# Kernel tuning notes

Measured on AMD Instinct MI355X. Metric: run time of the kernel, lower is better.

Reference implementation:

```python
import jax, jax.numpy as jnp
import numpy as np

LAT_MIN, LAT_MAX = -90.0, 90.0
LON_MIN, LON_MAX = 0.0, 360.0
N_LEVELS = 4
N_FEAT = 2
FINEST = 0.25
BASE = 1.0
LAT_SHAPE, LON_SHAPE = 720, 1440
GEODESIC_WEIGHT = True
TABLE = (LAT_SHAPE + 1) * (LON_SHAPE + 1)  # 1038961
# corner offsets in the torch BOX_OFFSETS order: (0,0),(0,1),(1,0),(1,1)
OFFS = np.array([[0, 0], [0, 1], [1, 0], [1, 1]], dtype=np.int32)


def setup_inputs() -> dict:
    key = jax.random.key(0)
    k1, k2 = jax.random.split(key)
    B = 2_000_000
    u = jax.random.uniform(k1, (B, 2), dtype=jnp.float32)
    # lat in [-90, 90), lon in [0, 360)
    x = jnp.stack([u[:, 0] * 180.0 - 90.0, u[:, 1] * 360.0], axis=1)
    embeddings = jax.random.uniform(k2, (N_LEVELS, TABLE, N_FEAT),
                                    minval=-1e-4, maxval=1e-4, dtype=jnp.float32)
    return {"x": x, "embeddings": embeddings}


def _geodesic(lat1, lon1, lat2, lon2):
    r = jnp.pi / 180.0
    rl1, rl2 = lat1 * r, lat2 * r
    dlat = (lat2 - lat1) * r
    dlon = (lon2 - lon1) * r
    a = jnp.sin(dlat / 2) ** 2 + jnp.cos(rl1) * jnp.cos(rl2) * jnp.sin(dlon / 2) ** 2
    return 2.0 * jnp.arctan2(jnp.sqrt(a), jnp.sqrt(1.0 - a))


def reference(x, embeddings):
    box_min = jnp.array([LAT_MIN - FINEST, LON_MIN - FINEST], dtype=x.dtype)
    box_max = jnp.array([LAT_MAX + FINEST, LON_MAX + FINEST], dtype=x.dtype)
    xc = jnp.clip(x, box_min, box_max)  # clamped coords used for grid indexing
    offs = jnp.asarray(OFFS)
    outs = []
    for i in range(N_LEVELS):
        gs = BASE * (2.0 ** i)  # grid size (same for lat and lon)
        bl = jnp.floor((xc - box_min) / gs).astype(jnp.int32)  # [B,2] bottom-left idx
        gmin = bl.astype(x.dtype) * gs + box_min                # [B,2]
        gmax = gmin + gs
        width = int(np.floor(LON_SHAPE / gs))
        # 4 corner flat indices: lat_idx * width + lon_idx -> [B,4]
        idx = (bl[:, 0:1] + offs[None, :, 0]) * width + (bl[:, 1:2] + offs[None, :, 1])
        e = embeddings[i][idx]  # gather: [B,4,F]
        if GEODESIC_WEIGHT:
            wlat = _geodesic(gmin[:, 0], gmin[:, 1], x[:, 0], gmin[:, 1]) / \
                   _geodesic(gmin[:, 0], gmin[:, 1], gmax[:, 0], gmin[:, 1])
            wlon = _geodesic(gmin[:, 0], x[:, 1], gmin[:, 0], gmax[:, 1]) / \
                   _geodesic(gmin[:, 0], gmin[:, 1], gmin[:, 0], gmax[:, 1])
        else:
            w = (x - gmin) / (gmax - gmin)
            wlat, wlon = w[:, 0], w[:, 1]
        # bilinear blend (corner order: 0=(0,0) 1=(0,1) 2=(1,0) 3=(1,1))
        c0 = e[:, 0] * (1 - wlat[:, None]) + e[:, 2] * wlat[:, None]
        c1 = e[:, 1] * (1 - wlat[:, None]) + e[:, 3] * wlat[:, None]
        outs.append(c0 * (1 - wlon[:, None]) + c1 * wlon[:, None])
    return jnp.concatenate(outs, axis=-1)  # [B, N_LEVELS*N_FEAT]
```

## Files before the change

kernel.cpp:

```cpp
#include <hip/hip_runtime.h>
#include <hip/hip_fp16.h>

#define NT 256

constexpr int TABLE_SZ = 721 * 1441;

constexpr int QLAT = 181, QLON = 361;
constexpr int NCELLS = QLAT * QLON;

constexpr int LUT_OFF0 = 0, LUT_OFF1 = 181, LUT_OFF2 = 272, LUT_OFF3 = 318;
constexpr int LUT_N = 341;

typedef float v4f __attribute__((ext_vector_type(4)));
typedef float v2f __attribute__((ext_vector_type(2)));

__device__ __constant__ float c_s2_tab[4] = {0.008726535498f, 0.017452406437f,
                                             0.034899496703f, 0.069756473744f};

__global__ __launch_bounds__(256)
void build_superquad(const float* __restrict__ emb, uint4* __restrict__ sq)
{
    int c = blockIdx.x * 256 + threadIdx.x;
    if (c >= NCELLS) return;
    int la = c / QLON, lo = c - la * QLON;
    const float2* embv = (const float2*)emb;
    #pragma unroll
    for (int i = 0; i < 4; ++i) {
        const int width = 1440 >> i;
        const int ra = la >> i, co = lo >> i;
        const float2* t = embv + (size_t)i * TABLE_SZ;
        float2 e0 = t[ra * width + co];
        float2 e1 = t[ra * width + co + 1];
        float2 e2 = t[(ra + 1) * width + co];
        float2 e3 = t[(ra + 1) * width + co + 1];
        union { uint4 u; __half2 h[4]; } pk;
        pk.h[0] = __floats2half2_rn(e0.x, e0.y);
        pk.h[1] = __floats2half2_rn(e1.x, e1.y);
        pk.h[2] = __floats2half2_rn(e2.x, e2.y);
        pk.h[3] = __floats2half2_rn(e3.x, e3.y);
        sq[(size_t)c * 4 + i] = pk.u;
    }
}

template <bool USE_SQ>
__global__ __launch_bounds__(NT)
void ngp_interp_kernel(const float* __restrict__ x,
                       const float* __restrict__ emb,
                       const uint4* __restrict__ sq,
                       float* __restrict__ out,
                       int B)
{
    const float r = 0.017453292519943295f;
    const float bmin_lat = -90.25f;
    const float bmin_lon = -0.25f;

    __shared__ float2 lut[LUT_N];
    for (int t = threadIdx.x; t < LUT_N; t += NT) {
        int lvl, row;
        if (t < LUT_OFF1)      { lvl = 0; row = t; }
        else if (t < LUT_OFF2) { lvl = 1; row = t - LUT_OFF1; }
        else if (t < LUT_OFF3) { lvl = 2; row = t - LUT_OFF2; }
        else                   { lvl = 3; row = t - LUT_OFF3; }
        const float gs = (float)(1 << lvl);
        const float gmin_lat = (float)row * gs + bmin_lat;
        const float ca = fabsf(__cosf(gmin_lat * r));
        const float z2 = ca * c_s2_tab[lvl];
        const float n2 = z2 + z2 * z2 * z2 * (1.0f / 6.0f);
        lut[t] = make_float2(ca, __builtin_amdgcn_rcpf(n2));
    }
    __syncthreads();

    const int p = blockIdx.x * NT + threadIdx.x;
    if (p >= B) return;

    const v2f xp = __builtin_nontemporal_load(reinterpret_cast<const v2f*>(x) + p);
    const float xlat = xp.x;
    const float xlon = xp.y;

    const float bmax_lat = 90.25f, bmax_lon = 360.25f;
    const float xc_lat = fminf(fmaxf(xlat, bmin_lat), bmax_lat);
    const float xc_lon = fminf(fmaxf(xlon, bmin_lon), bmax_lon);

    const float v_lat = xc_lat - bmin_lat;
    const float v_lon = xc_lon - bmin_lon;

    const int cell0 = (int)floorf(v_lat) * QLON + (int)floorf(v_lon);
    const uint4* cellp = sq + (size_t)cell0 * 4;

    const int lut_off[4] = {LUT_OFF0, LUT_OFF1, LUT_OFF2, LUT_OFF3};

    float o[8];

    #pragma unroll
    for (int i = 0; i < 4; ++i) {
        const float gs     = (float)(1 << i);
        const float inv_gs = 1.0f / gs;
        const int   width  = 1440 >> i;

        const float blat_f = floorf(v_lat * inv_gs);
        const float blon_f = floorf(v_lon * inv_gs);
        const float gmin_lat = blat_f * gs + bmin_lat;
        const float gmin_lon = blon_f * gs + bmin_lon;
        const float gmax_lon = gmin_lon + gs;
        const int bl_lat = (int)blat_f;

        v2f E0, E1, E2, E3;
        if (USE_SQ) {
            union { uint4 u; __half2 h[4]; } pk;
            pk.u = cellp[i];
            float2 f0 = __half22float2(pk.h[0]);
            float2 f1 = __half22float2(pk.h[1]);
            float2 f2 = __half22float2(pk.h[2]);
            float2 f3 = __half22float2(pk.h[3]);
            E0 = (v2f){f0.x, f0.y}; E1 = (v2f){f1.x, f1.y};
            E2 = (v2f){f2.x, f2.y}; E3 = (v2f){f3.x, f3.y};
        } else {
            const int bl_lon = (int)blon_f;
            const int idx00 = bl_lat * width + bl_lon;
            const float* base0 = emb + ((size_t)i * TABLE_SZ + (size_t)idx00) * 2;
            const float* base1 = base0 + (size_t)width * 2;
            v4f eA, eB;
            __builtin_memcpy(&eA, base0, 16);
            __builtin_memcpy(&eB, base1, 16);
            E0 = (v2f){eA.x, eA.y}; E1 = (v2f){eA.z, eA.w};
            E2 = (v2f){eB.x, eB.y}; E3 = (v2f){eB.z, eB.w};
        }

        const float wlat = (xlat - gmin_lat) * inv_gs;

        const float2 cl = lut[lut_off[i] + bl_lat];
        const float h1 = (gmax_lon - xlon) * r * 0.5f;
        const float s1 = h1 - h1 * h1 * h1 * (1.0f / 6.0f);
        const float z1 = cl.x * s1;
        const float n1 = z1 + z1 * z1 * z1 * (1.0f / 6.0f);
        const float wlon = n1 * cl.y;

        const v2f wa = {wlat, wlat};
        const v2f wo = {wlon, wlon};
        const v2f c0 = E0 + (E2 - E0) * wa;
        const v2f c1 = E1 + (E3 - E1) * wa;
        const v2f res = c0 + (c1 - c0) * wo;
        o[2*i]   = res.x;
        o[2*i+1] = res.y;
    }

    v4f* op = reinterpret_cast<v4f*>(out + (size_t)p * 8);
    v4f lo = {o[0], o[1], o[2], o[3]};
    v4f hi = {o[4], o[5], o[6], o[7]};
    __builtin_nontemporal_store(lo, op);
    __builtin_nontemporal_store(hi, op + 1);
}

extern "C" void kernel_launch(void* const* d_in, const int* in_sizes, int n_in,
                              void* d_out, int out_size, void* d_ws, size_t ws_size,
                              hipStream_t stream)
{
    const float* x   = (const float*)d_in[0];
    const float* emb = (const float*)d_in[1];
    float* out = (float*)d_out;
    const int B = in_sizes[0] / 2;
    const int grid = (B + NT - 1) / NT;

    const size_t sq_bytes = (size_t)NCELLS * 64;
    if (ws_size >= sq_bytes) {
        uint4* sq = (uint4*)d_ws;
        build_superquad<<<(NCELLS + 255) / 256, 256, 0, stream>>>(emb, sq);
        ngp_interp_kernel<true><<<grid, NT, 0, stream>>>(x, emb, sq, out, B);
    } else {
        ngp_interp_kernel<false><<<grid, NT, 0, stream>>>(x, emb, nullptr, out, B);
    }
}
```

Before: 123.3 us.

## Process two points per thread and parallelize superquad build per level

The build kernel now uses one thread per (cell, level) pair instead of looping over four levels per cell, so writes are coalesced across consecutive threads and there are more threads to work with. The main kernel handles two points per thread: it issues all eight 16-byte superquad loads up front for more memory-level parallelism, halves the number of blocks and the shared LUT setup per point, and writes four vector stores per thread. The old templated fallback is split out into its own kernel that computes the cosines inline. The trade-off is higher register pressure and a requirement that B be even.

```diff
diff --git a/kernel.cpp b/kernel.cpp
--- a/kernel.cpp
+++ b/kernel.cpp
@@ -20,32 +20,28 @@
 __global__ __launch_bounds__(256)
 void build_superquad(const float* __restrict__ emb, uint4* __restrict__ sq)
 {
-    int c = blockIdx.x * 256 + threadIdx.x;
-    if (c >= NCELLS) return;
-    int la = c / QLON, lo = c - la * QLON;
-    const float2* embv = (const float2*)emb;
-    #pragma unroll
-    for (int i = 0; i < 4; ++i) {
-        const int width = 1440 >> i;
-        const int ra = la >> i, co = lo >> i;
-        const float2* t = embv + (size_t)i * TABLE_SZ;
-        float2 e0 = t[ra * width + co];
-        float2 e1 = t[ra * width + co + 1];
-        float2 e2 = t[(ra + 1) * width + co];
-        float2 e3 = t[(ra + 1) * width + co + 1];
-        union { uint4 u; __half2 h[4]; } pk;
-        pk.h[0] = __floats2half2_rn(e0.x, e0.y);
-        pk.h[1] = __floats2half2_rn(e1.x, e1.y);
-        pk.h[2] = __floats2half2_rn(e2.x, e2.y);
-        pk.h[3] = __floats2half2_rn(e3.x, e3.y);
-        sq[(size_t)c * 4 + i] = pk.u;
-    }
-}
-
-template <bool USE_SQ>
+    int t = blockIdx.x * 256 + threadIdx.x;
+    if (t >= NCELLS * 4) return;
+    const int c = t >> 2;
+    const int i = t & 3;
+    const int la = c / QLON, lo = c - la * QLON;
+    const int width = 1440 >> i;
+    const int ra = la >> i, co = lo >> i;
+    const float2* tb = (const float2*)emb + (size_t)i * TABLE_SZ;
+    float2 e0 = tb[ra * width + co];
+    float2 e1 = tb[ra * width + co + 1];
+    float2 e2 = tb[(ra + 1) * width + co];
+    float2 e3 = tb[(ra + 1) * width + co + 1];
+    union { uint4 u; __half2 h[4]; } pk;
+    pk.h[0] = __floats2half2_rn(e0.x, e0.y);
+    pk.h[1] = __floats2half2_rn(e1.x, e1.y);
+    pk.h[2] = __floats2half2_rn(e2.x, e2.y);
+    pk.h[3] = __floats2half2_rn(e3.x, e3.y);
+    sq[t] = pk.u;
+}
+
 __global__ __launch_bounds__(NT)
 void ngp_interp_kernel(const float* __restrict__ x,
-                       const float* __restrict__ emb,
                        const uint4* __restrict__ sq,
                        float* __restrict__ out,
                        int B)
@@ -70,80 +66,127 @@
     }
     __syncthreads();
 
+    const int p0 = (blockIdx.x * NT + threadIdx.x) * 2;
+    if (p0 >= B) return;
+
+    const v4f xp = __builtin_nontemporal_load(
+        reinterpret_cast<const v4f*>(x) + (p0 >> 1));
+    const float xla[2] = {xp.x, xp.z};
+    const float xlo[2] = {xp.y, xp.w};
+
+    const float bmax_lat = 90.25f, bmax_lon = 360.25f;
+
+    float vla[2], vlo[2];
+    uint4 q[2][4];
+    #pragma unroll
+    for (int k = 0; k < 2; ++k) {
+        const float xc_lat = fminf(fmaxf(xla[k], bmin_lat), bmax_lat);
+        const float xc_lon = fminf(fmaxf(xlo[k], bmin_lon), bmax_lon);
+        vla[k] = xc_lat - bmin_lat;
+        vlo[k] = xc_lon - bmin_lon;
+        const int cell0 = (int)floorf(vla[k]) * QLON + (int)floorf(vlo[k]);
+        const uint4* cellp = sq + (size_t)cell0 * 4;
+        #pragma unroll
+        for (int i = 0; i < 4; ++i) q[k][i] = cellp[i];
+    }
+
+    float o[16];
+
+    #pragma unroll
+    for (int k = 0; k < 2; ++k) {
+        #pragma unroll
+        for (int i = 0; i < 4; ++i) {
+            const float gs     = (float)(1 << i);
+            const float inv_gs = 1.0f / gs;
+            const int   loff   = (i == 0) ? LUT_OFF0 : (i == 1) ? LUT_OFF1
+                                 : (i == 2) ? LUT_OFF2 : LUT_OFF3;
+
+            const float blat_f = floorf(vla[k] * inv_gs);
+            const float blon_f = floorf(vlo[k] * inv_gs);
+            const float gmin_lat = blat_f * gs + bmin_lat;
+            const float gmin_lon = blon_f * gs + bmin_lon;
+            const float gmax_lon = gmin_lon + gs;
+            const int bl_lat = (int)blat_f;
+
+            union { uint4 u; __half2 h[4]; } pk;
+            pk.u = q[k][i];
+            const float2 f0 = __half22float2(pk.h[0]);
+            const float2 f1 = __half22float2(pk.h[1]);
+            const float2 f2 = __half22float2(pk.h[2]);
+            const float2 f3 = __half22float2(pk.h[3]);
+
+            const float wlat = (xla[k] - gmin_lat) * inv_gs;
+
+            const float2 cl = lut[loff + bl_lat];
+            const float h1 = (gmax_lon - xlo[k]) * r * 0.5f;
+            const float s1 = h1 - h1 * h1 * h1 * (1.0f / 6.0f);
+            const float z1 = cl.x * s1;
+            const float n1 = z1 + z1 * z1 * z1 * (1.0f / 6.0f);
+            const float wlon = n1 * cl.y;
+
+            const float c0x = f0.x + (f2.x - f0.x) * wlat;
+            const float c0y = f0.y + (f2.y - f0.y) * wlat;
+            const float c1x = f1.x + (f3.x - f1.x) * wlat;
+            const float c1y = f1.y + (f3.y - f1.y) * wlat;
+            o[k * 8 + 2 * i]     = c0x + (c1x - c0x) * wlon;
+            o[k * 8 + 2 * i + 1] = c0y + (c1y - c0y) * wlon;
+        }
+    }
+
+    v4f* op = reinterpret_cast<v4f*>(out + (size_t)p0 * 8);
+    #pragma unroll
+    for (int j = 0; j < 4; ++j) {
+        v4f v = {o[4 * j], o[4 * j + 1], o[4 * j + 2], o[4 * j + 3]};
+        __builtin_nontemporal_store(v, op + j);
+    }
+}
+
+__global__ __launch_bounds__(NT)
+void ngp_interp_fallback(const float* __restrict__ x,
+                         const float* __restrict__ emb,
+                         float* __restrict__ out,
+                         int B)
+{
     const int p = blockIdx.x * NT + threadIdx.x;
     if (p >= B) return;
-
-    const v2f xp = __builtin_nontemporal_load(reinterpret_cast<const v2f*>(x) + p);
-    const float xlat = xp.x;
-    const float xlon = xp.y;
-
-    const float bmax_lat = 90.25f, bmax_lon = 360.25f;
+    const float xlat = x[(size_t)p * 2], xlon = x[(size_t)p * 2 + 1];
+    const float bmin_lat = -90.25f, bmax_lat = 90.25f;
+    const float bmin_lon = -0.25f,  bmax_lon = 360.25f;
     const float xc_lat = fminf(fmaxf(xlat, bmin_lat), bmax_lat);
     const float xc_lon = fminf(fmaxf(xlon, bmin_lon), bmax_lon);
-
-    const float v_lat = xc_lat - bmin_lat;
-    const float v_lon = xc_lon - bmin_lon;
-
-    const int cell0 = (int)floorf(v_lat) * QLON + (int)floorf(v_lon);
-    const uint4* cellp = sq + (size_t)cell0 * 4;
-
-    const int lut_off[4] = {LUT_OFF0, LUT_OFF1, LUT_OFF2, LUT_OFF3};
-
+    const float r = 0.017453292519943295f;
     float o[8];
-
     #pragma unroll
     for (int i = 0; i < 4; ++i) {
-        const float gs     = (float)(1 << i);
-        const float inv_gs = 1.0f / gs;
-        const int   width  = 1440 >> i;
-
-        const float blat_f = floorf(v_lat * inv_gs);
-        const float blon_f = floorf(v_lon * inv_gs);
+        const float gs = (float)(1 << i), inv_gs = 1.0f / gs;
+        const int width = 1440 >> i;
+        const float blat_f = floorf((xc_lat - bmin_lat) * inv_gs);
+        const float blon_f = floorf((xc_lon - bmin_lon) * inv_gs);
         const float gmin_lat = blat_f * gs + bmin_lat;
         const float gmin_lon = blon_f * gs + bmin_lon;
         const float gmax_lon = gmin_lon + gs;
-        const int bl_lat = (int)blat_f;
-
-        v2f E0, E1, E2, E3;
-        if (USE_SQ) {
-            union { uint4 u; __half2 h[4]; } pk;
-            pk.u = cellp[i];
-            float2 f0 = __half22float2(pk.h[0]);
-            float2 f1 = __half22float2(pk.h[1]);
-            float2 f2 = __half22float2(pk.h[2]);
-            float2 f3 = __half22float2(pk.h[3]);
-            E0 = (v2f){f0.x, f0.y}; E1 = (v2f){f1.x, f1.y};
-            E2 = (v2f){f2.x, f2.y}; E3 = (v2f){f3.x, f3.y};
-        } else {
-            const int bl_lon = (int)blon_f;
-            const int idx00 = bl_lat * width + bl_lon;
-            const float* base0 = emb + ((size_t)i * TABLE_SZ + (size_t)idx00) * 2;
-            const float* base1 = base0 + (size_t)width * 2;
-            v4f eA, eB;
-            __builtin_memcpy(&eA, base0, 16);
-            __builtin_memcpy(&eB, base1, 16);
-            E0 = (v2f){eA.x, eA.y}; E1 = (v2f){eA.z, eA.w};
-            E2 = (v2f){eB.x, eB.y}; E3 = (v2f){eB.z, eB.w};
-        }
-
+        const int idx00 = (int)blat_f * width + (int)blon_f;
+        const float* base0 = emb + ((size_t)i * TABLE_SZ + (size_t)idx00) * 2;
+        const float* base1 = base0 + (size_t)width * 2;
+        v4f eA, eB;
+        __builtin_memcpy(&eA, base0, 16);
+        __builtin_memcpy(&eB, base1, 16);
         const float wlat = (xlat - gmin_lat) * inv_gs;
-
-        const float2 cl = lut[lut_off[i] + bl_lat];
+        const float ca = fabsf(__cosf(gmin_lat * r));
         const float h1 = (gmax_lon - xlon) * r * 0.5f;
         const float s1 = h1 - h1 * h1 * h1 * (1.0f / 6.0f);
-        const float z1 = cl.x * s1;
+        const float z1 = ca * s1;
+        const float z2 = ca * c_s2_tab[i];
         const float n1 = z1 + z1 * z1 * z1 * (1.0f / 6.0f);
-        const float wlon = n1 * cl.y;
-
-        const v2f wa = {wlat, wlat};
-        const v2f wo = {wlon, wlon};
-        const v2f c0 = E0 + (E2 - E0) * wa;
-        const v2f c1 = E1 + (E3 - E1) * wa;
-        const v2f res = c0 + (c1 - c0) * wo;
-        o[2*i]   = res.x;
-        o[2*i+1] = res.y;
-    }
-
+        const float n2 = z2 + z2 * z2 * z2 * (1.0f / 6.0f);
+        const float wlon = n1 * __builtin_amdgcn_rcpf(n2);
+        const float c0x = eA.x + (eB.x - eA.x) * wlat;
+        const float c0y = eA.y + (eB.y - eA.y) * wlat;
+        const float c1x = eA.z + (eB.z - eA.z) * wlat;
+        const float c1y = eA.w + (eB.w - eA.w) * wlat;
+        o[2*i]   = c0x + (c1x - c0x) * wlon;
+        o[2*i+1] = c0y + (c1y - c0y) * wlon;
+    }
     v4f* op = reinterpret_cast<v4f*>(out + (size_t)p * 8);
     v4f lo = {o[0], o[1], o[2], o[3]};
     v4f hi = {o[4], o[5], o[6], o[7]};
@@ -159,14 +202,14 @@
     const float* emb = (const float*)d_in[1];
     float* out = (float*)d_out;
     const int B = in_sizes[0] / 2;
-    const int grid = (B + NT - 1) / NT;
 
     const size_t sq_bytes = (size_t)NCELLS * 64;
-    if (ws_size >= sq_bytes) {
+    if (ws_size >= sq_bytes && (B % 2) == 0) {
         uint4* sq = (uint4*)d_ws;
-        build_superquad<<<(NCELLS + 255) / 256, 256, 0, stream>>>(emb, sq);
-        ngp_interp_kernel<true><<<grid, NT, 0, stream>>>(x, emb, sq, out, B);
+        build_superquad<<<(NCELLS * 4 + 255) / 256, 256, 0, stream>>>(emb, sq);
+        const int npair = B / 2;
+        ngp_interp_kernel<<<(npair + NT - 1) / NT, NT, 0, stream>>>(x, sq, out, B);
     } else {
-        ngp_interp_kernel<false><<<grid, NT, 0, stream>>>(x, emb, nullptr, out, B);
-    }
-}
+        ngp_interp_fallback<<<(B + NT - 1) / NT, NT, 0, stream>>>(x, emb, out, B);
+    }
+}
```

Result: slower. 135.7 us (+10.1%).
